# Kernel tuning notes

Hardware: AMD Instinct MI355X
Metric: run time of the kernel (lower is better)

The kernel has to match this reference:

```python
import jax, jax.numpy as jnp
import numpy as np

NEIGHBORS = 16  # init kwarg 'neighbors'


def _mlp(x, params):
    # SetTransform with reduction='none': pointwise MLP, ReLU between layers, linear output
    for W, b in params[:-1]:
        x = jax.nn.relu(x @ W + b)
    W, b = params[-1]
    return x @ W + b


def setup_inputs() -> dict:
    key = jax.random.key(0)
    B, K, P, DIM, C_IN = 4, 2048, 4096, 3, 64
    C_MID, C_OUT = 32, 128
    WH = 32          # weight_hidden sizes
    FH = 256         # final_hidden size
    FIN = C_IN * C_MID  # 2048, final_conv input

    ks = jax.random.split(key, 16)

    def lin(k, fan_in, fan_out):
        k1, k2 = jax.random.split(k)
        s = 1.0 / np.sqrt(fan_in)
        W = jax.random.uniform(k1, (fan_in, fan_out), minval=-s, maxval=s, dtype=jnp.float32)
        b = jax.random.uniform(k2, (fan_out,), minval=-s, maxval=s, dtype=jnp.float32)
        return W, b

    wc0_W, wc0_b = lin(ks[0], DIM, WH)
    wc1_W, wc1_b = lin(ks[1], WH, WH)
    wc2_W, wc2_b = lin(ks[2], WH, C_MID)
    fc0_W, fc0_b = lin(ks[3], FIN, FH)
    fc1_W, fc1_b = lin(ks[4], FH, C_OUT)

    return {
        "keys": jax.random.normal(ks[5], (B, K, DIM), dtype=jnp.float32),
        "points": jax.random.normal(ks[6], (B, P, DIM), dtype=jnp.float32),
        "feats": jax.random.normal(ks[7], (B, P, C_IN), dtype=jnp.float32),
        "wc0_W": wc0_W, "wc0_b": wc0_b,
        "wc1_W": wc1_W, "wc1_b": wc1_b,
        "wc2_W": wc2_W, "wc2_b": wc2_b,
        "fc0_W": fc0_W, "fc0_b": fc0_b,
        "fc1_W": fc1_W, "fc1_b": fc1_b,
    }


def reference(keys, points, feats,
              wc0_W, wc0_b, wc1_W, wc1_b, wc2_W, wc2_b,
              fc0_W, fc0_b, fc1_W, fc1_b):
    B, K, _ = keys.shape
    # Euclidean dist_fn: rel_pos [B,K,P,dim], squared dist [B,K,P]; all points valid
    dist_vec = points[:, None, :, :] - keys[:, :, None, :]
    dist = jnp.sum(dist_vec * dist_vec, axis=-1)
    # k smallest distances -> neighbor indices [B,K,N]
    _, idxs = jax.lax.top_k(-dist, NEIGHBORS)
    # gather relative positions [B,K,N,dim] and neighbor features [B,K,N,c_in]
    neighbor_rel = jnp.take_along_axis(dist_vec, idxs[..., None], axis=2)
    b_idx = jnp.arange(B)[:, None, None]
    neighbor_feats = feats[b_idx, idxs]
    # per-edge weight MLP: [B,K,N,dim] -> [B,K,N,c_mid]
    m = _mlp(neighbor_rel, [(wc0_W, wc0_b), (wc1_W, wc1_b), (wc2_W, wc2_b)])
    # masked matmul aggregation (all neighbors valid under euclidean dist_fn):
    # m^T @ neighbor_feats -> [B,K,c_mid,c_in], flattened to [B,K,c_mid*c_in]
    e = jnp.einsum('bknm,bknc->bkmc', m, neighbor_feats).reshape(B, K, -1)
    # final pointwise MLP -> [B,K,c_out]
    return _mlp(e, [(fc0_W, fc0_b), (fc1_W, fc1_b)])
```

## Files before the change

### kernel.cpp

```cpp
#include <hip/hip_runtime.h>
#include <cfloat>
#include <climits>

#define BATCH 4
#define KQ    2048
#define NP    4096
#define CIN   64
#define CMID  32
#define NB    16
#define NBINS 4096
#define CANDCAP 256
#define QPB   4

typedef short   bf16x8  __attribute__((ext_vector_type(8)));
typedef float   floatx4 __attribute__((ext_vector_type(4)));

__device__ __forceinline__ unsigned short f2bf(float f) {
  unsigned u = __float_as_uint(f);
  u = (u + 0x7fffu + ((u >> 16) & 1u)) >> 16;
  return (unsigned short)u;
}
__device__ __forceinline__ float bf2f(unsigned short u) {
  return __uint_as_float((unsigned)u << 16);
}

__device__ __forceinline__ void load_lds16(const void* g, void* l) {
  __builtin_amdgcn_global_load_lds(
      (const __attribute__((address_space(1))) unsigned int*)g,
      (__attribute__((address_space(3))) unsigned int*)l, 16, 0, 0);
}

__global__ __launch_bounds__(256, 8) void select_topk(
    const float* __restrict__ keys, const float* __restrict__ points,
    int* __restrict__ nidx_g) {
  __shared__ __align__(16) int hist[NBINS];
  __shared__ int   psum[256];
  __shared__ float cand_d[CANDCAP];
  __shared__ int   cand_i[CANDCAP];
  __shared__ int   nidx[NB];
  __shared__ int   sel_cnt, cand_cnt, sBin, sCbelow;

  const int tid = threadIdx.x;
  const int b   = blockIdx.x >> 11;

#pragma unroll
  for (int t = 0; t < 4; ++t)
    *reinterpret_cast<int4*>(&hist[(tid + t * 256) * 4]) = int4{0, 0, 0, 0};
  if (tid == 0) { sel_cnt = 0; cand_cnt = 0; }

  const float kx = keys[blockIdx.x * 3 + 0];
  const float ky = keys[blockIdx.x * 3 + 1];
  const float kz = keys[blockIdx.x * 3 + 2];
  __syncthreads();

  const float4* pv =
      reinterpret_cast<const float4*>(points + (size_t)b * NP * 3) + (size_t)tid * 12;
  float dreg[16];
#pragma unroll
  for (int g = 0; g < 4; ++g) {
    const float4 v0 = pv[g * 3 + 0];
    const float4 v1 = pv[g * 3 + 1];
    const float4 v2 = pv[g * 3 + 2];
    const float px[4] = {v0.x, v0.w, v1.z, v2.y};
    const float py[4] = {v0.y, v1.x, v1.w, v2.z};
    const float pz[4] = {v0.z, v1.y, v2.x, v2.w};
#pragma unroll
    for (int j = 0; j < 4; ++j) {
      const float dx = px[j] - kx, dy = py[j] - ky, dz = pz[j] - kz;
      const float d  = dx * dx + dy * dy + dz * dz;
      dreg[g * 4 + j] = d;
      atomicAdd(&hist[__float_as_uint(d) >> 19], 1);
    }
  }
  __syncthreads();

  {
    const int base = tid * 16;
    int s = 0;
#pragma unroll
    for (int t = 0; t < 4; ++t) {
      const int4 hv = *reinterpret_cast<const int4*>(&hist[base + t * 4]);
      s += hv.x + hv.y + hv.z + hv.w;
    }
    psum[tid] = s;
  }
  __syncthreads();

  if (tid < 64) {
    const int q = psum[tid * 4] + psum[tid * 4 + 1] + psum[tid * 4 + 2] + psum[tid * 4 + 3];
    int incl = q;
#pragma unroll
    for (int off = 1; off < 64; off <<= 1) {
      int u = __shfl_up(incl, off);
      if (tid >= off) incl += u;
    }
    unsigned long long bal = __ballot(incl >= NB);
    int firstlane = __ffsll((long long)bal) - 1;
    if (tid == firstlane) {
      int cum = incl - q;
      int bin = -1;
      for (int t = 0; t < 4 && bin < 0; ++t) {
        const int ps = psum[tid * 4 + t];
        if (cum + ps >= NB) {
          const int b0 = (tid * 4 + t) * 16;
          for (int j = 0; j < 16; ++j) {
            const int h = hist[b0 + j];
            if (cum + h >= NB) { bin = b0 + j; break; }
            cum += h;
          }
        } else cum += ps;
      }
      sBin = bin; sCbelow = cum;
    }
  }
  __syncthreads();

  const unsigned B = (unsigned)sBin;
#pragma unroll
  for (int j = 0; j < 16; ++j) {
    const int i = tid * 16 + j;
    const unsigned bk = __float_as_uint(dreg[j]) >> 19;
    if (bk < B) {
      int pos = atomicAdd(&sel_cnt, 1);
      nidx[pos] = i;
    } else if (bk == B) {
      int pos = atomicAdd(&cand_cnt, 1);
      if (pos < CANDCAP) { cand_d[pos] = dreg[j]; cand_i[pos] = i; }
    }
  }
  __syncthreads();

  {
    const int rem = NB - sCbelow;
    const int cc  = min(cand_cnt, CANDCAP);
    for (int j = tid; j < cc; j += 256) {
      const float dj = cand_d[j]; const int ij = cand_i[j];
      int rank = 0;
      for (int k = 0; k < cc; ++k) {
        const float dk = cand_d[k]; const int ik = cand_i[k];
        rank += (dk < dj || (dk == dj && ik < ij)) ? 1 : 0;
      }
      if (rank < rem) nidx[sCbelow + rank] = ij;
    }
  }
  __syncthreads();

  if (tid < NB) nidx_g[blockIdx.x * NB + tid] = nidx[tid];
}

__global__ __launch_bounds__(256) void edge_prep(
    const float* __restrict__ keys, const float* __restrict__ points,
    const float* __restrict__ feats, const int* __restrict__ nidx_g,
    const float* __restrict__ wc0_W, const float* __restrict__ wc0_b,
    const float* __restrict__ wc1_W, const float* __restrict__ wc1_b,
    const float* __restrict__ wc2_W, const float* __restrict__ wc2_b,
    const float* __restrict__ fc0_W, const float* __restrict__ fc1_W,
    unsigned short* __restrict__ W0T, unsigned short* __restrict__ W1T,
    unsigned short* __restrict__ E) {
  __shared__ __align__(16) char smem[4 * 5888];
  float (*tt)[33] = reinterpret_cast<float(*)[33]>(smem);

  const int tid = threadIdx.x;
  const int bid = blockIdx.x;
  const int q0  = bid * QPB;

  if (bid < 544) {
    const float* W; unsigned short* WT; int K, N, k0, n0;
    if (bid < 512) { W = fc0_W; WT = W0T; K = 2048; N = 256;
                     k0 = (bid >> 3) * 32; n0 = (bid & 7) * 32; }
    else           { W = fc1_W; WT = W1T; K = 256;  N = 128;
                     k0 = ((bid - 512) >> 2) * 32; n0 = ((bid - 512) & 3) * 32; }
    const int tx = tid & 31, ty = tid >> 5;
#pragma unroll
    for (int p = 0; p < 4; ++p)
      tt[ty + p * 8][tx] = W[(size_t)(k0 + ty + p * 8) * N + n0 + tx];
    __syncthreads();
#pragma unroll
    for (int p = 0; p < 4; ++p)
      WT[(size_t)(n0 + ty + p * 8) * K + k0 + tx] = f2bf(tt[tx][ty + p * 8]);
    __syncthreads();
  }

  const int wv   = tid >> 6, lane = tid & 63;
  const int s    = lane & 15, g = lane >> 4;
  const int q    = q0 + wv;
  const int b    = q >> 11;

  unsigned short* h2s = reinterpret_cast<unsigned short*>(smem + wv * 5888);
  unsigned short* ms  = reinterpret_cast<unsigned short*>(smem + wv * 5888 + 1280);
  unsigned short* fsT = reinterpret_cast<unsigned short*>(smem + wv * 5888 + 2816);

  bf16x8 B1[2], B2[2];
#pragma unroll
  for (int t = 0; t < 2; ++t) {
#pragma unroll
    for (int e = 0; e < 8; ++e) {
      const int k = 8 * g + e, c = s + 16 * t;
      B1[t][e] = (short)f2bf(wc1_W[k * 32 + c]);
      B2[t][e] = (short)f2bf(wc2_W[k * 32 + c]);
    }
  }

  const int idx = nidx_g[q * NB + s];
  const float* p = points + ((size_t)b * NP + idx) * 3;
  const float kx = keys[q * 3], ky = keys[q * 3 + 1], kz = keys[q * 3 + 2];
  const float rx = p[0] - kx, ry = p[1] - ky, rz = p[2] - kz;
  bf16x8 A1;
#pragma unroll
  for (int e = 0; e < 8; ++e) {
    const int j = 8 * g + e;
    float h = rx * wc0_W[j] + ry * wc0_W[32 + j] + rz * wc0_W[64 + j] + wc0_b[j];
    A1[e] = (short)f2bf(fmaxf(h, 0.f));
  }

  const floatx4 zc = {0.f, 0.f, 0.f, 0.f};

#pragma unroll
  for (int t = 0; t < 2; ++t) {
    floatx4 d = __builtin_amdgcn_mfma_f32_16x16x32_bf16(A1, B1[t], zc, 0, 0, 0);
    const float bv = wc1_b[s + 16 * t];
#pragma unroll
    for (int r = 0; r < 4; ++r)
      h2s[(g * 4 + r) * 40 + 16 * t + s] = f2bf(fmaxf(d[r] + bv, 0.f));
  }

  const bf16x8 A2 = *reinterpret_cast<const bf16x8*>(&h2s[s * 40 + g * 8]);

#pragma unroll
  for (int t = 0; t < 2; ++t) {
    floatx4 d = __builtin_amdgcn_mfma_f32_16x16x32_bf16(A2, B2[t], zc, 0, 0, 0);
    const float bv = wc2_b[s + 16 * t];
    ushort4 o;
    o.x = f2bf(d[0] + bv); o.y = f2bf(d[1] + bv);
    o.z = f2bf(d[2] + bv); o.w = f2bf(d[3] + bv);
    *reinterpret_cast<ushort4*>(&ms[(16 * t + s) * 24 + g * 4]) = o;
  }

#pragma unroll
  for (int t = 0; t < 4; ++t) {
    const int chunk = g + 4 * t;
    const int n = s;
    const int idx_n = nidx_g[q * NB + n];
    const float4 v = *reinterpret_cast<const float4*>(
        feats + ((size_t)b * NP + idx_n) * CIN + chunk * 4);
    fsT[(chunk * 4 + 0) * 24 + n] = f2bf(v.x);
    fsT[(chunk * 4 + 1) * 24 + n] = f2bf(v.y);
    fsT[(chunk * 4 + 2) * 24 + n] = f2bf(v.z);
    fsT[(chunk * 4 + 3) * 24 + n] = f2bf(v.w);
  }

  bf16x8 fA[4], mB[2];
  const bf16x8 zf = {};
  if (lane < 32) {
#pragma unroll
    for (int ct = 0; ct < 4; ++ct)
      fA[ct] = *reinterpret_cast<const bf16x8*>(&fsT[(ct * 16 + s) * 24 + g * 8]);
#pragma unroll
    for (int mt = 0; mt < 2; ++mt)
      mB[mt] = *reinterpret_cast<const bf16x8*>(&ms[(mt * 16 + s) * 24 + g * 8]);
  } else {
#pragma unroll
    for (int ct = 0; ct < 4; ++ct) fA[ct] = zf;
#pragma unroll
    for (int mt = 0; mt < 2; ++mt) mB[mt] = zf;
  }

  unsigned short* Eq = E + (size_t)q * 2048;
#pragma unroll
  for (int mt = 0; mt < 2; ++mt) {
#pragma unroll
    for (int ct = 0; ct < 4; ++ct) {
      floatx4 d = __builtin_amdgcn_mfma_f32_16x16x32_bf16(fA[ct], mB[mt], zc, 0, 0, 0);
      ushort4 o;
      o.x = f2bf(d[0]); o.y = f2bf(d[1]); o.z = f2bf(d[2]); o.w = f2bf(d[3]);
      *reinterpret_cast<ushort4*>(&Eq[(16 * mt + s) * 64 + ct * 16 + g * 4]) = o;
    }
  }
}

template <int KDIM, bool RELU, bool OUTBF16, bool SWIZZLE>
__global__ __launch_bounds__(256) void gemm_mfma(
    const unsigned short* __restrict__ A,
    const unsigned short* __restrict__ Bt,
    const float* __restrict__ bias,
    void* __restrict__ Cout, int ldc) {
  __shared__ __align__(16) unsigned short Al[2][64 * 128];
  __shared__ __align__(16) unsigned short Bl[2][64 * 128];
  const int tid  = threadIdx.x;
  int m0, n0;
  if (SWIZZLE) {
    const int L    = blockIdx.x;
    const int slot = L >> 3;
    m0 = ((L & 7) * 16 + (slot >> 2)) * 64;
    n0 = (slot & 3) * 64;
  } else {
    m0 = blockIdx.x * 64;
    n0 = blockIdx.y * 64;
  }
  const int wv   = tid >> 6, lane = tid & 63;
  const int quad = lane >> 4, s = lane & 15;
  const int moff = (wv & 1) * 32, noff = (wv >> 1) * 32;
  const int lr   = lane >> 4, lc = lane & 15;

  floatx4 acc[2][2] = {{{0.f,0.f,0.f,0.f},{0.f,0.f,0.f,0.f}},
                       {{0.f,0.f,0.f,0.f},{0.f,0.f,0.f,0.f}}};

  auto stage = [&](int buf, int k0) {
#pragma unroll
    for (int t = 0; t < 4; ++t) {
      const int R0 = wv * 16 + t * 4;
      const int r  = R0 + lr;
      const int gc = lc ^ (r & 7);
      load_lds16(A  + (size_t)(m0 + r) * KDIM + k0 + gc * 8, &Al[buf][R0 * 128]);
      load_lds16(Bt + (size_t)(n0 + r) * KDIM + k0 + gc * 8, &Bl[buf][R0 * 128]);
    }
  };

  auto compute = [&](int buf) {
#pragma unroll
    for (int h = 0; h < 4; ++h) {
      bf16x8 af[2], bfr[2];
#pragma unroll
      for (int i = 0; i < 2; ++i) {
        const int r = moff + i * 16 + s;
        af[i] = *reinterpret_cast<const bf16x8*>(
            &Al[buf][(size_t)r * 128 + ((((h << 2) | quad) ^ (r & 7)) << 3)]);
      }
#pragma unroll
      for (int j = 0; j < 2; ++j) {
        const int r = noff + j * 16 + s;
        bfr[j] = *reinterpret_cast<const bf16x8*>(
            &Bl[buf][(size_t)r * 128 + ((((h << 2) | quad) ^ (r & 7)) << 3)]);
      }
#pragma unroll
      for (int i = 0; i < 2; ++i)
#pragma unroll
        for (int j = 0; j < 2; ++j)
          acc[i][j] = __builtin_amdgcn_mfma_f32_16x16x32_bf16(af[i], bfr[j], acc[i][j], 0, 0, 0);
    }
  };

  constexpr int NT = KDIM / 128;

  stage(0, 0);
  __syncthreads();
  int cur = 0;
#pragma unroll 1
  for (int it = 0; it < NT - 1; ++it) {
    stage(cur ^ 1, (it + 1) * 128);
    compute(cur);
    __syncthreads();
    cur ^= 1;
  }
  compute(cur);

#pragma unroll
  for (int i = 0; i < 2; ++i)
#pragma unroll
    for (int j = 0; j < 2; ++j) {
      const int col = n0 + noff + j * 16 + s;
      const float bv = bias[col];
#pragma unroll
      for (int r = 0; r < 4; ++r) {
        const int row = m0 + moff + i * 16 + quad * 4 + r;
        float v = acc[i][j][r] + bv;
        if (RELU) v = fmaxf(v, 0.f);
        if (OUTBF16)
          ((unsigned short*)Cout)[(size_t)row * ldc + col] = f2bf(v);
        else
          ((float*)Cout)[(size_t)row * ldc + col] = v;
      }
    }
}

extern "C" void kernel_launch(void* const* d_in, const int* in_sizes, int n_in,
                              void* d_out, int out_size, void* d_ws, size_t ws_size,
                              hipStream_t stream) {
  const float* keys   = (const float*)d_in[0];
  const float* points = (const float*)d_in[1];
  const float* feats  = (const float*)d_in[2];
  const float* wc0_W  = (const float*)d_in[3];
  const float* wc0_b  = (const float*)d_in[4];
  const float* wc1_W  = (const float*)d_in[5];
  const float* wc1_b  = (const float*)d_in[6];
  const float* wc2_W  = (const float*)d_in[7];
  const float* wc2_b  = (const float*)d_in[8];
  const float* fc0_W  = (const float*)d_in[9];
  const float* fc0_b  = (const float*)d_in[10];
  const float* fc1_W  = (const float*)d_in[11];
  const float* fc1_b  = (const float*)d_in[12];
  float* out = (float*)d_out;

  const int M = BATCH * KQ;
  char* ws = (char*)d_ws;
  unsigned short* E    = (unsigned short*)(ws);
  unsigned short* H16  = (unsigned short*)(ws + (size_t)33554432);
  unsigned short* W0T  = (unsigned short*)(ws + (size_t)37748736);
  unsigned short* W1T  = (unsigned short*)(ws + (size_t)38797312);
  int*            nidx = (int*)(ws + (size_t)38862848);

  select_topk<<<M, 256, 0, stream>>>(keys, points, nidx);
  edge_prep<<<M / QPB, 256, 0, stream>>>(keys, points, feats, nidx,
                                         wc0_W, wc0_b, wc1_W, wc1_b, wc2_W, wc2_b,
                                         fc0_W, fc1_W, W0T, W1T, E);
  gemm_mfma<2048, true,  true,  true ><<<512, 256, 0, stream>>>(E, W0T, fc0_b, H16, 256);
  gemm_mfma<256,  false, false, false><<<dim3(M / 64, 2), 256, 0, stream>>>(H16, W1T, fc1_b, out, 128);
}
```

Before: 160.6 us.

## Run top-k selection with one wavefront per query and packed 16-bit histogram

Restructures the top-k selection kernel so each 64-lane wavefront handles a whole query instead of a 256-thread block per query. The 4096-bin histogram is packed into 2048 32-bit words, with two 16-bit counters per word and a transposed layout. Bin search becomes two wave-level prefix scans with no block barriers, and results go straight to global memory. This removes __syncthreads and block-level LDS traffic per query. In exchange each lane holds 64 distances in registers and does strided, uncoalesced scalar point loads, which may raise register pressure and lower occupancy.

```diff
diff --git a/kernel.cpp b/kernel.cpp
--- a/kernel.cpp
+++ b/kernel.cpp
@@ -8,9 +8,9 @@
 #define CIN   64
 #define CMID  32
 #define NB    16
-#define NBINS 4096
 #define CANDCAP 256
 #define QPB   4
+#define TQW   4
 
 typedef short   bf16x8  __attribute__((ext_vector_type(8)));
 typedef float   floatx4 __attribute__((ext_vector_type(4)));
@@ -30,122 +30,98 @@
       (__attribute__((address_space(3))) unsigned int*)l, 16, 0, 0);
 }
 
-__global__ __launch_bounds__(256, 8) void select_topk(
+__global__ __launch_bounds__(256, 3) void select_topk(
     const float* __restrict__ keys, const float* __restrict__ points,
     int* __restrict__ nidx_g) {
-  __shared__ __align__(16) int hist[NBINS];
-  __shared__ int   psum[256];
-  __shared__ float cand_d[CANDCAP];
-  __shared__ int   cand_i[CANDCAP];
-  __shared__ int   nidx[NB];
-  __shared__ int   sel_cnt, cand_cnt, sBin, sCbelow;
-
-  const int tid = threadIdx.x;
-  const int b   = blockIdx.x >> 11;
-
-#pragma unroll
-  for (int t = 0; t < 4; ++t)
-    *reinterpret_cast<int4*>(&hist[(tid + t * 256) * 4]) = int4{0, 0, 0, 0};
-  if (tid == 0) { sel_cnt = 0; cand_cnt = 0; }
-
-  const float kx = keys[blockIdx.x * 3 + 0];
-  const float ky = keys[blockIdx.x * 3 + 1];
-  const float kz = keys[blockIdx.x * 3 + 2];
-  __syncthreads();
-
-  const float4* pv =
-      reinterpret_cast<const float4*>(points + (size_t)b * NP * 3) + (size_t)tid * 12;
-  float dreg[16];
-#pragma unroll
-  for (int g = 0; g < 4; ++g) {
-    const float4 v0 = pv[g * 3 + 0];
-    const float4 v1 = pv[g * 3 + 1];
-    const float4 v2 = pv[g * 3 + 2];
-    const float px[4] = {v0.x, v0.w, v1.z, v2.y};
-    const float py[4] = {v0.y, v1.x, v1.w, v2.z};
-    const float pz[4] = {v0.z, v1.y, v2.x, v2.w};
-#pragma unroll
-    for (int j = 0; j < 4; ++j) {
-      const float dx = px[j] - kx, dy = py[j] - ky, dz = pz[j] - kz;
-      const float d  = dx * dx + dy * dy + dz * dz;
-      dreg[g * 4 + j] = d;
-      atomicAdd(&hist[__float_as_uint(d) >> 19], 1);
-    }
-  }
-  __syncthreads();
-
-  {
-    const int base = tid * 16;
-    int s = 0;
-#pragma unroll
-    for (int t = 0; t < 4; ++t) {
-      const int4 hv = *reinterpret_cast<const int4*>(&hist[base + t * 4]);
-      s += hv.x + hv.y + hv.z + hv.w;
-    }
-    psum[tid] = s;
-  }
-  __syncthreads();
-
-  if (tid < 64) {
-    const int q = psum[tid * 4] + psum[tid * 4 + 1] + psum[tid * 4 + 2] + psum[tid * 4 + 3];
-    int incl = q;
-#pragma unroll
-    for (int off = 1; off < 64; off <<= 1) {
-      int u = __shfl_up(incl, off);
-      if (tid >= off) incl += u;
-    }
-    unsigned long long bal = __ballot(incl >= NB);
-    int firstlane = __ffsll((long long)bal) - 1;
-    if (tid == firstlane) {
-      int cum = incl - q;
-      int bin = -1;
-      for (int t = 0; t < 4 && bin < 0; ++t) {
-        const int ps = psum[tid * 4 + t];
-        if (cum + ps >= NB) {
-          const int b0 = (tid * 4 + t) * 16;
-          for (int j = 0; j < 16; ++j) {
-            const int h = hist[b0 + j];
-            if (cum + h >= NB) { bin = b0 + j; break; }
-            cum += h;
-          }
-        } else cum += ps;
-      }
-      sBin = bin; sCbelow = cum;
-    }
-  }
-  __syncthreads();
-
-  const unsigned B = (unsigned)sBin;
-#pragma unroll
-  for (int j = 0; j < 16; ++j) {
-    const int i = tid * 16 + j;
-    const unsigned bk = __float_as_uint(dreg[j]) >> 19;
-    if (bk < B) {
-      int pos = atomicAdd(&sel_cnt, 1);
-      nidx[pos] = i;
-    } else if (bk == B) {
-      int pos = atomicAdd(&cand_cnt, 1);
-      if (pos < CANDCAP) { cand_d[pos] = dreg[j]; cand_i[pos] = i; }
-    }
-  }
-  __syncthreads();
-
-  {
-    const int rem = NB - sCbelow;
-    const int cc  = min(cand_cnt, CANDCAP);
-    for (int j = tid; j < cc; j += 256) {
-      const float dj = cand_d[j]; const int ij = cand_i[j];
-      int rank = 0;
-      for (int k = 0; k < cc; ++k) {
-        const float dk = cand_d[k]; const int ik = cand_i[k];
-        rank += (dk < dj || (dk == dj && ik < ij)) ? 1 : 0;
-      }
-      if (rank < rem) nidx[sCbelow + rank] = ij;
-    }
-  }
-  __syncthreads();
-
-  if (tid < NB) nidx_g[blockIdx.x * NB + tid] = nidx[tid];
+  __shared__ unsigned hist[TQW][2048];
+  __shared__ float cand_d[TQW][CANDCAP];
+  __shared__ int   cand_i[TQW][CANDCAP];
+  __shared__ int   cnts[TQW][2];
+
+  const int tid  = threadIdx.x;
+  const int wv   = tid >> 6, lane = tid & 63;
+  const int q    = blockIdx.x * TQW + wv;
+  const int b    = q >> 11;
+
+  unsigned* h = hist[wv];
+#pragma unroll
+  for (int i = 0; i < 8; ++i)
+    *reinterpret_cast<uint4*>(&h[(i * 64 + lane) * 4]) = uint4{0, 0, 0, 0};
+  if (lane == 0) { cnts[wv][0] = 0; cnts[wv][1] = 0; }
+
+  const float kx = keys[q * 3 + 0];
+  const float ky = keys[q * 3 + 1];
+  const float kz = keys[q * 3 + 2];
+
+  const float* pb = points + (size_t)b * NP * 3;
+  float dreg[64];
+#pragma unroll
+  for (int i = 0; i < 64; ++i) {
+    const int pi = i * 64 + lane;
+    const float px = pb[pi * 3 + 0];
+    const float py = pb[pi * 3 + 1];
+    const float pz = pb[pi * 3 + 2];
+    const float dx = px - kx, dy = py - ky, dz = pz - kz;
+    const float d  = dx * dx + dy * dy + dz * dz;
+    dreg[i] = d;
+    const unsigned bits = __float_as_uint(d);
+    const unsigned w    = bits >> 20;
+    const unsigned addr = ((w & 31u) << 6) | (w >> 5);
+    atomicAdd(&h[addr], (bits & 0x80000u) ? 65536u : 1u);
+  }
+
+  int s = 0;
+#pragma unroll
+  for (int i = 0; i < 32; ++i) {
+    const unsigned w = h[(i << 6) | lane];
+    s += (int)(w & 0xffffu) + (int)(w >> 16);
+  }
+  int incl = s;
+#pragma unroll
+  for (int off = 1; off < 64; off <<= 1) {
+    const int u = __shfl_up(incl, off);
+    if (lane >= off) incl += u;
+  }
+  const unsigned long long bal = __ballot(incl >= NB);
+  const int bl = __ffsll((long long)bal) - 1;
+  const int cumbl = __shfl(incl, bl) - __shfl(s, bl);
+
+  const unsigned wb = h[(((unsigned)(lane >> 1)) << 6) | (unsigned)bl];
+  const int cb = (lane & 1) ? (int)(wb >> 16) : (int)(wb & 0xffffu);
+  int binc = cb;
+#pragma unroll
+  for (int off = 1; off < 64; off <<= 1) {
+    const int u = __shfl_up(binc, off);
+    if (lane >= off) binc += u;
+  }
+  const unsigned long long bal2 = __ballot(cumbl + binc >= NB);
+  const int bo = __ffsll((long long)bal2) - 1;
+  const unsigned Bbin = (unsigned)(bl * 64 + bo);
+  const int cbelow = cumbl + __shfl(binc, bo) - __shfl(cb, bo);
+
+#pragma unroll
+  for (int i = 0; i < 64; ++i) {
+    const unsigned bin = __float_as_uint(dreg[i]) >> 19;
+    if (bin < Bbin) {
+      const int pos = atomicAdd(&cnts[wv][0], 1);
+      nidx_g[q * NB + pos] = i * 64 + lane;
+    } else if (bin == Bbin) {
+      const int pos = atomicAdd(&cnts[wv][1], 1);
+      if (pos < CANDCAP) { cand_d[wv][pos] = dreg[i]; cand_i[wv][pos] = i * 64 + lane; }
+    }
+  }
+
+  const int cc  = min(cnts[wv][1], CANDCAP);
+  const int rem = NB - cbelow;
+  for (int j = lane; j < cc; j += 64) {
+    const float dj = cand_d[wv][j]; const int ij = cand_i[wv][j];
+    int rank = 0;
+    for (int k = 0; k < cc; ++k) {
+      const float dk = cand_d[wv][k]; const int ik = cand_i[wv][k];
+      rank += (dk < dj || (dk == dj && ik < ij)) ? 1 : 0;
+    }
+    if (rank < rem) nidx_g[q * NB + cbelow + rank] = ij;
+  }
 }
 
 __global__ __launch_bounds__(256) void edge_prep(
@@ -399,7 +375,7 @@
   unsigned short* W1T  = (unsigned short*)(ws + (size_t)38797312);
   int*            nidx = (int*)(ws + (size_t)38862848);
 
-  select_topk<<<M, 256, 0, stream>>>(keys, points, nidx);
+  select_topk<<<M / TQW, 256, 0, stream>>>(keys, points, nidx);
   edge_prep<<<M / QPB, 256, 0, stream>>>(keys, points, feats, nidx,
                                          wc0_W, wc0_b, wc1_W, wc1_b, wc2_W, wc2_b,
                                          fc0_W, fc1_W, W0T, W1T, E);
```

Result: slower. 202.3 us (+26.0%).
